# Performance work log

Hardware: AMD Instinct MI355X
Metric: run time of the kernel (lower is better)

Reference implementation:

```python
import jax, jax.numpy as jnp
import numpy as np

N_LEVELS = 16
MIN_RES = 16
MAX_RES = 512
N_ENC = 2 ** 14          # n_encodings (power of two)
E = 2                    # n_embed_dims
D = 3                    # n_input_dims
INIT_SCALE = 1e-4
B = 2 ** 21
_PRIMES = (1, 2654435761, 805459861)  # instant-NGP spatial hash primes


def _compute_resolutions():
    g = np.exp((np.log(MAX_RES) - np.log(MIN_RES)) / (N_LEVELS - 1))
    return [int(np.floor(MIN_RES * g ** l)) for l in range(N_LEVELS)]

RES = _compute_resolutions()  # [16,20,25,32,40,50,64,80,101,128,161,203,256,322,406,512]


def _level_features(x, table, res):
    """x:(B,3) in [-1,1], table:(E,N_ENC) -> (B,E).

    Equivalent to embmatrix[:, indices] densified to a (res,res,res) grid
    followed by F.grid_sample(mode='bilinear', padding_mode='zeros',
    align_corners=False), but computed per-corner on the fly (same math).
    """
    n = min(res ** D, N_ENC)
    # grid_sample align_corners=False unnormalization
    ix = ((x + 1.0) * res - 1.0) * 0.5            # (B,3) continuous voxel coords
    x0f = jnp.floor(ix)
    frac = ix - x0f                                # (B,3)
    x0 = x0f.astype(jnp.int32)
    tab_t = table.T                                # (N_ENC, E)
    feats = jnp.zeros((x.shape[0], E), dtype=x.dtype)
    for corner in range(2 ** D):
        off = jnp.array([(corner >> d) & 1 for d in range(D)], dtype=jnp.int32)
        c = x0 + off                               # (B,3) integer corner coords
        w = jnp.prod(jnp.where(off == 1, frac, 1.0 - frac), axis=-1)  # (B,) trilinear weight
        valid = jnp.all((c >= 0) & (c < res), axis=-1)                 # zero padding
        cc = jnp.clip(c, 0, res - 1).astype(jnp.uint32)
        if res ** D <= N_ENC:
            # direct (raveled) mapping: x fastest, matching indices[z,y,x]=f(x,y,z)
            idx = cc[:, 0] + cc[:, 1] * jnp.uint32(res) + cc[:, 2] * jnp.uint32(res * res)
        else:
            h = ((cc[:, 0] * jnp.uint32(_PRIMES[0]))
                 ^ (cc[:, 1] * jnp.uint32(_PRIMES[1]))
                 ^ (cc[:, 2] * jnp.uint32(_PRIMES[2])))
            idx = h & jnp.uint32(n - 1)
        g = tab_t[idx.astype(jnp.int32)]           # (B,E) gathered embeddings
        feats = feats + g * (w * valid)[:, None]
    return feats


def setup_inputs() -> dict:
    key = jax.random.key(0)
    kx, ke = jax.random.split(key)
    x = jax.random.uniform(kx, (B, D), dtype=jnp.float32, minval=-1.0, maxval=1.0)
    emb = jax.random.uniform(ke, (N_LEVELS, E, N_ENC), dtype=jnp.float32,
                             minval=-INIT_SCALE, maxval=INIT_SCALE)
    return {"x": x, "emb": emb}


def reference(x, emb):
    feats = [_level_features(x, emb[l], RES[l]) for l in range(N_LEVELS)]
    return jnp.stack(feats, axis=1)                # (B, L, E)
```

## Files before the change

kernel.cpp:

```cpp
#include <hip/hip_runtime.h>
#include <stdint.h>

#define NL  16
#define NE  16384
#define NB  64
#define BLK1 512
#define PPB  ((1 << 21) / NB)
#define ITER (PPB / BLK1)
#define BLK2 256
#define TP   512
#define BLKF 1024

constexpr int kRes[NL] = {16,20,25,32,40,50,64,80,101,128,161,203,256,322,406,512};
__device__ const int dRes[NL] = {16,20,25,32,40,50,64,80,101,128,161,203,256,322,406,512};

__global__ void pack_kernel(const float* __restrict__ emb, uint32_t* __restrict__ tbl) {
    int i = blockIdx.x * blockDim.x + threadIdx.x;
    if (i >= NL * NE) return;
    int l = i >> 14;
    int j = i & (NE - 1);
    float e0 = emb[(size_t)l * 2 * NE + j];
    float e1 = emb[(size_t)l * 2 * NE + NE + j];
    uint32_t u0 = __float_as_uint(e0); u0 = (u0 + 0x7fffu + ((u0 >> 16) & 1u)) >> 16;
    uint32_t u1 = __float_as_uint(e1); u1 = (u1 + 0x7fffu + ((u1 >> 16) & 1u)) >> 16;
    tbl[i] = u0 | (u1 << 16);
}

__global__ __launch_bounds__(BLK1, 4)
void level_kernel(const float* __restrict__ x, const uint32_t* __restrict__ tbl,
                  uint32_t* __restrict__ mid) {
    __shared__ __align__(16) uint32_t lds[NE];

    const int tid   = threadIdx.x;
    const int level = blockIdx.x & (NL - 1);
    const int chunk = blockIdx.x >> 4;

    {
        const uint4* g = (const uint4*)(tbl + ((size_t)level << 14));
        uint4* dst = (uint4*)lds;
        #pragma unroll
        for (int p = 0; p < 8; ++p) dst[p * BLK1 + tid] = g[p * BLK1 + tid];
    }
    __syncthreads();

    const int   res  = dRes[level];
    const float hres = 0.5f * (float)res;
    const float cadd = hres - 0.5f;
    const bool hashed = (res * res * res > NE);

    uint32_t* dst = mid + ((size_t)level << 21);
    const float3* xs = (const float3*)x;
    const size_t pbase = (size_t)chunk * PPB + tid;

    if (hashed) {
        float3 nxt = xs[pbase];
        for (int i = 0; i < ITER; ++i) {
            const float3 cur = nxt;
            if (i + 1 < ITER) nxt = xs[pbase + (size_t)(i + 1) * BLK1];
            const float pc[3] = {cur.x, cur.y, cur.z};

            float    w[3][2];
            uint32_t a[3][2];
            #pragma unroll
            for (int d = 0; d < 3; ++d) {
                constexpr uint32_t P[3] = {1u, 2654435761u, 805459861u};
                float ix = fmaf(pc[d], hres, cadd);
                float fl = floorf(ix);
                const float fr = ix - fl;
                const int lo = (int)fl;
                w[d][0] = (lo >= 0)       ? (1.0f - fr) : 0.0f;
                w[d][1] = (lo + 1 <= res - 1) ? fr      : 0.0f;
                a[d][0] = (uint32_t)lo * P[d];
                a[d][1] = a[d][0] + P[d];
            }

            float    wxy[4];
            uint32_t axy[4];
            #pragma unroll
            for (int c = 0; c < 4; ++c) {
                wxy[c] = w[0][c & 1] * w[1][(c >> 1) & 1];
                axy[c] = a[0][c & 1] ^ a[1][(c >> 1) & 1];
            }

            float f0 = 0.0f, f1 = 0.0f;
            #pragma unroll
            for (int c = 0; c < 8; ++c) {
                const int cxy = c & 3, bz = (c >> 2) & 1;
                const uint32_t idx = (axy[cxy] ^ a[2][bz]) & (uint32_t)(NE - 1);
                const float wt = wxy[cxy] * w[2][bz];
                const uint32_t v = lds[idx];
                f0 = fmaf(wt, __uint_as_float(v << 16),          f0);
                f1 = fmaf(wt, __uint_as_float(v & 0xffff0000u),  f1);
            }

            const uint32_t u0 = (__float_as_uint(f0) + 0x8000u) >> 16;
            const uint32_t u1 = (__float_as_uint(f1) + 0x8000u) & 0xffff0000u;
            dst[pbase + (size_t)i * BLK1] = u0 | u1;
        }
    } else {
        const uint32_t sy = (uint32_t)res, sz = (uint32_t)(res * res);
        float3 nxt = xs[pbase];
        for (int i = 0; i < ITER; ++i) {
            const float3 cur = nxt;
            if (i + 1 < ITER) nxt = xs[pbase + (size_t)(i + 1) * BLK1];
            const float pc[3] = {cur.x, cur.y, cur.z};

            float    w[3][2];
            uint32_t a[3][2];
            #pragma unroll
            for (int d = 0; d < 3; ++d) {
                const uint32_t stride = (d == 0) ? 1u : ((d == 1) ? sy : sz);
                float ix = fmaf(pc[d], hres, cadd);
                float fl = floorf(ix);
                const float fr = ix - fl;
                const int lo = (int)fl, hi = lo + 1;
                w[d][0] = (lo >= 0)       ? (1.0f - fr) : 0.0f;
                w[d][1] = (hi <= res - 1) ? fr          : 0.0f;
                const int loc = lo < 0 ? 0 : lo;
                const int hic = hi > res - 1 ? res - 1 : hi;
                a[d][0] = (uint32_t)loc * stride;
                a[d][1] = (uint32_t)hic * stride;
            }

            float    wxy[4];
            uint32_t axy[4];
            #pragma unroll
            for (int c = 0; c < 4; ++c) {
                wxy[c] = w[0][c & 1] * w[1][(c >> 1) & 1];
                axy[c] = a[0][c & 1] + a[1][(c >> 1) & 1];
            }

            float f0 = 0.0f, f1 = 0.0f;
            #pragma unroll
            for (int c = 0; c < 8; ++c) {
                const int cxy = c & 3, bz = (c >> 2) & 1;
                const uint32_t idx = axy[cxy] + a[2][bz];
                const float wt = wxy[cxy] * w[2][bz];
                const uint32_t v = lds[idx];
                f0 = fmaf(wt, __uint_as_float(v << 16),          f0);
                f1 = fmaf(wt, __uint_as_float(v & 0xffff0000u),  f1);
            }

            const uint32_t u0 = (__float_as_uint(f0) + 0x8000u) >> 16;
            const uint32_t u1 = (__float_as_uint(f1) + 0x8000u) & 0xffff0000u;
            dst[pbase + (size_t)i * BLK1] = u0 | u1;
        }
    }
}

__global__ __launch_bounds__(BLK2, 4)
void transpose_kernel(const uint32_t* __restrict__ mid, float* __restrict__ out) {
    __shared__ uint32_t t[TP * 17];

    const int tid = threadIdx.x;
    const size_t base_p = (size_t)blockIdx.x * TP;

    #pragma unroll
    for (int l = 0; l < NL; ++l) {
        const uint32_t* s = mid + ((size_t)l << 21) + base_p;
        t[tid * 17 + l]         = s[tid];
        t[(tid + 256) * 17 + l] = s[tid + 256];
    }
    __syncthreads();

    float4* o = (float4*)(out + base_p * 32);
    #pragma unroll
    for (int it = 0; it < 16; ++it) {
        const int f = it * BLK2 + tid;
        const int p = f >> 3, q = f & 7;
        const uint32_t v0 = t[p * 17 + 2 * q];
        const uint32_t v1 = t[p * 17 + 2 * q + 1];
        o[f] = make_float4(__uint_as_float(v0 << 16), __uint_as_float(v0 & 0xffff0000u),
                           __uint_as_float(v1 << 16), __uint_as_float(v1 & 0xffff0000u));
    }
}

__global__ __launch_bounds__(BLKF, 4)
void hashenc_kernel(const float* __restrict__ x, const uint32_t* __restrict__ tbl,
                    float* __restrict__ out) {
    __shared__ __align__(16) uint32_t lds[NE];

    const int tid  = threadIdx.x;
    const size_t b = (size_t)blockIdx.x * BLKF + tid;

    const float3 p3 = ((const float3*)x)[b];
    const float pc[3] = {p3.x, p3.y, p3.z};

    {
        const uint4* g = (const uint4*)tbl;
        uint4 r0 = g[0 * BLKF + tid], r1 = g[1 * BLKF + tid];
        uint4 r2 = g[2 * BLKF + tid], r3 = g[3 * BLKF + tid];
        uint4* dst = (uint4*)lds;
        dst[0 * BLKF + tid] = r0; dst[1 * BLKF + tid] = r1;
        dst[2 * BLKF + tid] = r2; dst[3 * BLKF + tid] = r3;
    }

    float acc[16];
    #pragma unroll
    for (int i = 0; i < 16; ++i) acc[i] = 0.0f;

    #pragma unroll
    for (int l = 0; l < NL; ++l) {
        __syncthreads();

        uint4 r0, r1, r2, r3;
        if (l + 1 < NL) {
            const uint4* g = (const uint4*)(tbl + ((size_t)(l + 1) << 14));
            r0 = g[0 * BLKF + tid]; r1 = g[1 * BLKF + tid];
            r2 = g[2 * BLKF + tid]; r3 = g[3 * BLKF + tid];
        }

        const int   res  = kRes[l];
        const float hres = 0.5f * (float)res;
        const float cadd = hres - 0.5f;
        const bool hashed = (res * res * res > NE);

        float fr[3]; int c0[3];
        #pragma unroll
        for (int d = 0; d < 3; ++d) {
            float ix = fmaf(pc[d], hres, cadd);
            float fl = floorf(ix);
            fr[d] = ix - fl;
            c0[d] = (int)fl;
        }

        float    w[3][2];
        uint32_t a[3][2];
        #pragma unroll
        for (int d = 0; d < 3; ++d) {
            const int lo = c0[d], hi = c0[d] + 1;
            w[d][0] = (lo >= 0)     ? (1.0f - fr[d]) : 0.0f;
            w[d][1] = (hi <= res-1) ? fr[d]          : 0.0f;
            const int loc = lo < 0 ? 0 : lo;
            const int hic = hi > res - 1 ? res - 1 : hi;
            if (hashed) {
                constexpr uint32_t P[3] = {1u, 2654435761u, 805459861u};
                a[d][0] = (uint32_t)loc * P[d];
                a[d][1] = (uint32_t)hic * P[d];
            } else {
                const uint32_t stride = (d == 0) ? 1u : ((d == 1) ? (uint32_t)res
                                                                  : (uint32_t)(res * res));
                a[d][0] = (uint32_t)loc * stride;
                a[d][1] = (uint32_t)hic * stride;
            }
        }

        float    wxy[4];
        uint32_t axy[4];
        #pragma unroll
        for (int c = 0; c < 4; ++c) {
            const int bx = c & 1, by = (c >> 1) & 1;
            wxy[c] = w[0][bx] * w[1][by];
            axy[c] = hashed ? (a[0][bx] ^ a[1][by]) : (a[0][bx] + a[1][by]);
        }

        float f0 = 0.0f, f1 = 0.0f;
        #pragma unroll
        for (int c = 0; c < 8; ++c) {
            const int cxy = c & 3, bz = (c >> 2) & 1;
            const uint32_t idx = hashed
                ? ((axy[cxy] ^ a[2][bz]) & (uint32_t)(NE - 1))
                : (axy[cxy] + a[2][bz]);
            const float wt = wxy[cxy] * w[2][bz];
            const uint32_t v = lds[idx];
            f0 = fmaf(wt, __uint_as_float(v << 16),          f0);
            f1 = fmaf(wt, __uint_as_float(v & 0xffff0000u),  f1);
        }
        acc[2 * (l & 7) + 0] = f0;
        acc[2 * (l & 7) + 1] = f1;

        if (l + 1 < NL) {
            __syncthreads();
            uint4* dst = (uint4*)lds;
            dst[0 * BLKF + tid] = r0; dst[1 * BLKF + tid] = r1;
            dst[2 * BLKF + tid] = r2; dst[3 * BLKF + tid] = r3;
        }

        if ((l & 7) == 7) {
            float4* o = (float4*)(out + b * 32 + (size_t)(l >> 3) * 16);
            o[0] = make_float4(acc[0],  acc[1],  acc[2],  acc[3]);
            o[1] = make_float4(acc[4],  acc[5],  acc[6],  acc[7]);
            o[2] = make_float4(acc[8],  acc[9],  acc[10], acc[11]);
            o[3] = make_float4(acc[12], acc[13], acc[14], acc[15]);
        }
    }
}

extern "C" void kernel_launch(void* const* d_in, const int* in_sizes, int n_in,
                              void* d_out, int out_size, void* d_ws, size_t ws_size,
                              hipStream_t stream) {
    const float* x   = (const float*)d_in[0];
    const float* emb = (const float*)d_in[1];
    float* out = (float*)d_out;

    uint32_t* tbl = (uint32_t*)d_ws;
    const size_t tbl_bytes = (size_t)NL * NE * 4;
    const size_t mid_bytes = (size_t)NL * (1 << 21) * 4;

    const int npack = NL * NE;
    pack_kernel<<<dim3((npack + 255) / 256), dim3(256), 0, stream>>>(emb, tbl);

    if (ws_size >= tbl_bytes + mid_bytes) {
        uint32_t* mid = tbl + (size_t)NL * NE;
        level_kernel<<<dim3(NL * NB), dim3(BLK1), 0, stream>>>(x, tbl, mid);
        transpose_kernel<<<dim3((1 << 21) / TP), dim3(BLK2), 0, stream>>>(mid, out);
    } else {
        hashenc_kernel<<<dim3((1 << 21) / BLKF), dim3(BLKF), 0, stream>>>(x, tbl, out);
    }
}
```

Baseline: 183.6 us.

## Fuse bf16 table packing into level kernel and use nontemporal memory ops

Removes the separate pack kernel launch: each level block now reads the fp32 embeddings directly and packs them to bf16 pairs while filling LDS. The level kernel's intermediate writes and the transpose kernel's loads and stores become nontemporal, and the transpose loads two uint32 values per thread in one vector load. The aim is to cut one launch plus the table round trip, and to reduce cache pollution from the large streaming buffers. In exchange, every block now does redundant fp32 reads and conversions of its level table, and the else-branch fallback now silently skips work if the workspace is too small.

```diff
diff --git a/kernel.cpp b/kernel.cpp
--- a/kernel.cpp
+++ b/kernel.cpp
@@ -11,8 +11,15 @@
 #define TP   512
 #define BLKF 1024
 
+typedef unsigned int uint2_v  __attribute__((ext_vector_type(2)));
+typedef float        float4_v __attribute__((ext_vector_type(4)));
 constexpr int kRes[NL] = {16,20,25,32,40,50,64,80,101,128,161,203,256,322,406,512};
 __device__ const int dRes[NL] = {16,20,25,32,40,50,64,80,101,128,161,203,256,322,406,512};
+
+__device__ __forceinline__ uint32_t bf16_rtne(float f) {
+    uint32_t u = __float_as_uint(f);
+    return (u + 0x7fffu + ((u >> 16) & 1u)) >> 16;
+}
 
 __global__ void pack_kernel(const float* __restrict__ emb, uint32_t* __restrict__ tbl) {
     int i = blockIdx.x * blockDim.x + threadIdx.x;
@@ -21,13 +28,11 @@
     int j = i & (NE - 1);
     float e0 = emb[(size_t)l * 2 * NE + j];
     float e1 = emb[(size_t)l * 2 * NE + NE + j];
-    uint32_t u0 = __float_as_uint(e0); u0 = (u0 + 0x7fffu + ((u0 >> 16) & 1u)) >> 16;
-    uint32_t u1 = __float_as_uint(e1); u1 = (u1 + 0x7fffu + ((u1 >> 16) & 1u)) >> 16;
-    tbl[i] = u0 | (u1 << 16);
+    tbl[i] = bf16_rtne(e0) | (bf16_rtne(e1) << 16);
 }
 
 __global__ __launch_bounds__(BLK1, 4)
-void level_kernel(const float* __restrict__ x, const uint32_t* __restrict__ tbl,
+void level_kernel(const float* __restrict__ x, const float* __restrict__ emb,
                   uint32_t* __restrict__ mid) {
     __shared__ __align__(16) uint32_t lds[NE];
 
@@ -36,10 +41,20 @@
     const int chunk = blockIdx.x >> 4;
 
     {
-        const uint4* g = (const uint4*)(tbl + ((size_t)level << 14));
+        const float4* e0s = (const float4*)(emb + (size_t)level * 2 * NE);
+        const float4* e1s = (const float4*)(emb + (size_t)level * 2 * NE + NE);
         uint4* dst = (uint4*)lds;
         #pragma unroll
-        for (int p = 0; p < 8; ++p) dst[p * BLK1 + tid] = g[p * BLK1 + tid];
+        for (int p = 0; p < 8; ++p) {
+            const float4 a = e0s[p * BLK1 + tid];
+            const float4 b = e1s[p * BLK1 + tid];
+            uint4 v;
+            v.x = bf16_rtne(a.x) | (bf16_rtne(b.x) << 16);
+            v.y = bf16_rtne(a.y) | (bf16_rtne(b.y) << 16);
+            v.z = bf16_rtne(a.z) | (bf16_rtne(b.z) << 16);
+            v.w = bf16_rtne(a.w) | (bf16_rtne(b.w) << 16);
+            dst[p * BLK1 + tid] = v;
+        }
     }
     __syncthreads();
 
@@ -95,7 +110,7 @@
 
             const uint32_t u0 = (__float_as_uint(f0) + 0x8000u) >> 16;
             const uint32_t u1 = (__float_as_uint(f1) + 0x8000u) & 0xffff0000u;
-            dst[pbase + (size_t)i * BLK1] = u0 | u1;
+            __builtin_nontemporal_store(u0 | u1, &dst[pbase + (size_t)i * BLK1]);
         }
     } else {
         const uint32_t sy = (uint32_t)res, sz = (uint32_t)(res * res);
@@ -143,7 +158,7 @@
 
             const uint32_t u0 = (__float_as_uint(f0) + 0x8000u) >> 16;
             const uint32_t u1 = (__float_as_uint(f1) + 0x8000u) & 0xffff0000u;
-            dst[pbase + (size_t)i * BLK1] = u0 | u1;
+            __builtin_nontemporal_store(u0 | u1, &dst[pbase + (size_t)i * BLK1]);
         }
     }
 }
@@ -157,21 +172,26 @@
 
     #pragma unroll
     for (int l = 0; l < NL; ++l) {
-        const uint32_t* s = mid + ((size_t)l << 21) + base_p;
-        t[tid * 17 + l]         = s[tid];
-        t[(tid + 256) * 17 + l] = s[tid + 256];
+        const uint2_v* s = (const uint2_v*)(mid + ((size_t)l << 21) + base_p);
+        const uint2_v v = __builtin_nontemporal_load(&s[tid]);
+        t[(2 * tid) * 17 + l]     = v.x;
+        t[(2 * tid + 1) * 17 + l] = v.y;
     }
     __syncthreads();
 
-    float4* o = (float4*)(out + base_p * 32);
+    float4_v* o = (float4_v*)(out + base_p * 32);
     #pragma unroll
     for (int it = 0; it < 16; ++it) {
         const int f = it * BLK2 + tid;
         const int p = f >> 3, q = f & 7;
         const uint32_t v0 = t[p * 17 + 2 * q];
         const uint32_t v1 = t[p * 17 + 2 * q + 1];
-        o[f] = make_float4(__uint_as_float(v0 << 16), __uint_as_float(v0 & 0xffff0000u),
-                           __uint_as_float(v1 << 16), __uint_as_float(v1 & 0xffff0000u));
+        float4_v val;
+        val.x = __uint_as_float(v0 << 16);
+        val.y = __uint_as_float(v0 & 0xffff0000u);
+        val.z = __uint_as_float(v1 << 16);
+        val.w = __uint_as_float(v1 & 0xffff0000u);
+        __builtin_nontemporal_store(val, &o[f]);
     }
 }
 
@@ -293,18 +313,17 @@
     const float* emb = (const float*)d_in[1];
     float* out = (float*)d_out;
 
-    uint32_t* tbl = (uint32_t*)d_ws;
+    const size_t mid_bytes = (size_t)NL * (1 << 21) * 4;
     const size_t tbl_bytes = (size_t)NL * NE * 4;
-    const size_t mid_bytes = (size_t)NL * (1 << 21) * 4;
-
-    const int npack = NL * NE;
-    pack_kernel<<<dim3((npack + 255) / 256), dim3(256), 0, stream>>>(emb, tbl);
-
-    if (ws_size >= tbl_bytes + mid_bytes) {
-        uint32_t* mid = tbl + (size_t)NL * NE;
-        level_kernel<<<dim3(NL * NB), dim3(BLK1), 0, stream>>>(x, tbl, mid);
+
+    if (ws_size >= mid_bytes) {
+        uint32_t* mid = (uint32_t*)d_ws;
+        level_kernel<<<dim3(NL * NB), dim3(BLK1), 0, stream>>>(x, emb, mid);
         transpose_kernel<<<dim3((1 << 21) / TP), dim3(BLK2), 0, stream>>>(mid, out);
-    } else {
+    } else if (ws_size >= tbl_bytes) {
+        uint32_t* tbl = (uint32_t*)d_ws;
+        const int npack = NL * NE;
+        pack_kernel<<<dim3((npack + 255) / 256), dim3(256), 0, stream>>>(emb, tbl);
         hashenc_kernel<<<dim3((1 << 21) / BLKF), dim3(BLKF), 0, stream>>>(x, tbl, out);
     }
 }
```

Measured after the change: 172.9 us. 5.8% less time.
